# Kernel tuning notes

Hardware: AMD Instinct MI355X
Metric: run time of the kernel (lower is better)

## Reference

```python
import jax, jax.numpy as jnp
import numpy as np

B, P, M, C = 128, 8732, 16, 3
THRESHOLD, NEG_POS_RATIO, ALPHA = 0.5, 3, 1.0


def xy_to_cxcy(xy):
    return jnp.concatenate([(xy[..., 2:] + xy[..., :2]) / 2.0, xy[..., 2:] - xy[..., :2]], axis=-1)


def cxcy_to_xy(cxcy):
    return jnp.concatenate([cxcy[..., :2] - cxcy[..., 2:] / 2.0, cxcy[..., :2] + cxcy[..., 2:] / 2.0], axis=-1)


def cxcy_to_gcxgcy(cxcy, priors_cxcy):
    return jnp.concatenate([
        (cxcy[..., :2] - priors_cxcy[..., :2]) / (priors_cxcy[..., 2:] / 10.0),
        jnp.log(cxcy[..., 2:] / priors_cxcy[..., 2:]) * 5.0], axis=-1)


def jaccard(a, b):
    # a: (M,4) xyxy, b: (P,4) xyxy -> (M,P) IoU
    lt = jnp.maximum(a[:, None, :2], b[None, :, :2])
    rb = jnp.minimum(a[:, None, 2:], b[None, :, 2:])
    wh = jnp.clip(rb - lt, 0.0)
    inter = wh[..., 0] * wh[..., 1]
    area_a = (a[:, 2] - a[:, 0]) * (a[:, 3] - a[:, 1])
    area_b = (b[:, 2] - b[:, 0]) * (b[:, 3] - b[:, 1])
    return inter / (area_a[:, None] + area_b[None, :] - inter)


def setup_inputs() -> dict:
    key = jax.random.key(0)
    k1, k2, k3, k4, k5, k6 = jax.random.split(key, 6)
    predicted_locs = jax.random.normal(k1, (B, P, 4), dtype=jnp.float32)
    predicted_scores = jax.random.normal(k2, (B, P, C), dtype=jnp.float32)
    xy = jax.random.uniform(k3, (B, M, 2), minval=0.0, maxval=0.7)
    wh = jax.random.uniform(k4, (B, M, 2), minval=0.05, maxval=0.3)
    boxes = jnp.concatenate([xy, xy + wh], axis=-1).astype(jnp.float32)
    labels = jax.random.randint(k5, (B, M), 1, 4)  # classes {1,2,3}
    pc = jax.random.uniform(k6, (P, 2), minval=0.0, maxval=1.0)
    pwh = jax.random.uniform(jax.random.fold_in(k6, 1), (P, 2), minval=0.05, maxval=0.5)
    priors_cxcy = jnp.concatenate([pc, pwh], axis=-1).astype(jnp.float32)
    return {"predicted_locs": predicted_locs, "predicted_scores": predicted_scores,
            "boxes": boxes, "labels": labels, "priors_cxcy": priors_cxcy}


def _match_one(boxes_i, labels_i, priors_xy, priors_cxcy):
    ov = jaccard(boxes_i, priors_xy)                # (M, P)
    ov_prior = ov.max(axis=0)                       # best overlap per prior
    obj_prior = ov.argmax(axis=0)                   # best object per prior
    prior_obj = ov.argmax(axis=1)                   # best prior per object
    n_obj = boxes_i.shape[0]
    obj_prior = obj_prior.at[prior_obj].set(jnp.arange(n_obj))
    ov_prior = ov_prior.at[prior_obj].set(1.0)
    lab = jnp.where(ov_prior < THRESHOLD, 0, labels_i[obj_prior])
    tl = cxcy_to_gcxgcy(xy_to_cxcy(boxes_i[obj_prior]), priors_cxcy)
    return tl, lab


def reference(predicted_locs, predicted_scores, boxes, labels, priors_cxcy):
    priors_xy = cxcy_to_xy(priors_cxcy)
    true_locs, true_classes = jax.vmap(_match_one, in_axes=(0, 0, None, None))(
        boxes, labels, priors_xy, priors_cxcy)      # (B,P,4), (B,P)
    positive = true_classes > 0                      # (B,P)
    n_pos = positive.sum(axis=1)                     # (B,)
    n_pos_total = n_pos.sum()

    # localization loss: L1Loss (mean over selected positive elements)
    l1 = jnp.abs(predicted_locs - true_locs).sum(axis=-1)   # (B,P)
    loc_loss = jnp.where(n_pos_total > 0,
                         (l1 * positive).sum() / (4.0 * jnp.maximum(n_pos_total, 1).astype(jnp.float32)),
                         0.0)

    # multi-label one-hot targets (classes 1,2,3; 3 = pair -> targets cols 1&2)
    tc = true_classes.reshape(-1)
    ignore = tc == -1
    pair = tc == 3
    target = jax.nn.one_hot(tc + 1, 5, dtype=predicted_scores.dtype)[:, 1:4]  # (B*P,3)
    target = target.at[:, 1].set(jnp.where(pair, 1.0, target[:, 1]))
    target = target.at[:, 2].set(jnp.where(pair, 1.0, target[:, 2]))

    # BCEWithLogits, summed over classes
    logits = predicted_scores.reshape(-1, C)
    bce = (jnp.logaddexp(0.0, logits) - logits * target).sum(axis=1)  # (B*P,)
    conf_all = jnp.where(ignore, 0.0, bce).reshape(true_classes.shape)  # (B,P)

    conf_pos = (conf_all * positive).sum()
    conf_neg = jnp.where(positive, 0.0, conf_all)
    conf_neg_sorted = -jnp.sort(-conf_neg, axis=1)   # descending per row
    ranks = jnp.arange(P)[None, :]
    hard_neg = ranks < (NEG_POS_RATIO * n_pos)[:, None]
    conf_hard_neg = (conf_neg_sorted * hard_neg).sum()

    conf_loss = (conf_hard_neg + conf_pos) / (1e-10 + n_pos_total.astype(jnp.float32))
    total = conf_loss + ALPHA * loc_loss
    return total, conf_loss, loc_loss, n_pos
```

## Files before the change

kernel.cpp:

```cpp
#include <hip/hip_runtime.h>
#include <hip/hip_fp16.h>
#include <cstdint>
#include <cmath>

#define B_ 128
#define P_ 8732
#define QU_ 2183
#define M_ 16
#define NT 1024
#define NW 16
#define TAIL_ (QU_ - 2*NT)
#define PSTRIDE 9216
#define NFV 144
#define NSLOT 16

__device__ __forceinline__ float softplusf(float x) {
    float e = __builtin_amdgcn_exp2f(fabsf(x) * -1.44269504f);
    return fmaxf(x, 0.0f) + 0.69314718f * __builtin_amdgcn_logf(1.0f + e);
}

__device__ __forceinline__ float wred_sum_f(float v) {
#pragma unroll
    for (int o = 32; o > 0; o >>= 1) v += __shfl_down(v, o, 64);
    return v;
}
__device__ __forceinline__ int wred_sum_i(int v) {
#pragma unroll
    for (int o = 32; o > 0; o >>= 1) v += __shfl_down(v, o, 64);
    return v;
}

__device__ __forceinline__ void phaseD(
    int r, int p, float bv, int bm, float4 pr,
    float x0, float x1, float x2,
    const float* s_boxes, const int* s_labels,
    const float* __restrict__ plocs,
    unsigned short* __restrict__ bcew,
    int& np, float& cp, float& ls)
{
    bool pos = bv >= 0.5f;
    int lab = pos ? s_labels[bm] : 0;
    float t0 = (lab == 0) ? 1.0f : 0.0f;
    float t1 = (lab == 1 || lab == 3) ? 1.0f : 0.0f;
    float t2 = (lab == 2 || lab == 3) ? 1.0f : 0.0f;
    float bce = (softplusf(x0) - x0*t0) + (softplusf(x1) - x1*t1) + (softplusf(x2) - x2*t2);
    float hb = 0.0f;
    if (pos) {
        np++; cp += bce;
        float4 bb = ((const float4*)s_boxes)[bm];
        float cx = (bb.x + bb.z) * 0.5f, cy = (bb.y + bb.w) * 0.5f;
        float w = bb.z - bb.x, hh = bb.w - bb.y;
        float g0 = (cx - pr.x) / (pr.z * 0.1f);
        float g1 = (cy - pr.y) / (pr.w * 0.1f);
        float g2 = logf(w / pr.z) * 5.0f;
        float g3 = logf(hh / pr.w) * 5.0f;
        float4 pl = ((const float4*)plocs)[(size_t)r * P_ + p];
        ls += fabsf(pl.x - g0) + fabsf(pl.y - g1) + fabsf(pl.z - g2) + fabsf(pl.w - g3);
    } else {
        hb = bce;
    }
    bcew[(size_t)r * PSTRIDE + p] = __half_as_ushort(__float2half(hb));
}

__global__ __launch_bounds__(NT) void mbox_match_kernel(
    const float* __restrict__ plocs,
    const float* __restrict__ pscores,
    const float* __restrict__ boxes,
    const int*   __restrict__ labels,
    const float* __restrict__ priors,
    unsigned short* __restrict__ bcew,
    int2* __restrict__ cand,
    float* __restrict__ pcf, float* __restrict__ plc, int* __restrict__ pnp,
    unsigned int* __restrict__ gz)
{
    __shared__ float s_boxes[M_ * 4];
    __shared__ float s_area[M_];
    __shared__ int   s_labels[M_];
    __shared__ unsigned long long s_obj[M_ * NSLOT];
    __shared__ float s_pf[2 * NW];
    __shared__ int   s_pi[NW];

    const int bk = blockIdx.x;
    const int r  = bk >> 2;
    const int q  = bk & 3;
    const int tid = threadIdx.x;
    const int lane = tid & 63;
    const int wid = tid >> 6;
    const int p0 = q * QU_;

    if (bk == 0 && tid < 4) gz[tid] = 0u;

    const int  pA = p0 + tid;
    const int  pB = pA + NT;
    const bool cok = tid < TAIL_;
    const int  pC = cok ? (pB + NT) : pA;

    float4 prA = ((const float4*)priors)[pA];
    float4 prB = ((const float4*)priors)[pB];
    float4 prC = ((const float4*)priors)[pC];

    const float* scA = pscores + ((size_t)r * P_ + pA) * 3;
    const float* scB = pscores + ((size_t)r * P_ + pB) * 3;
    const float* scC = pscores + ((size_t)r * P_ + pC) * 3;
    float xA0 = scA[0], xA1 = scA[1], xA2 = scA[2];
    float xB0 = scB[0], xB1 = scB[1], xB2 = scB[2];
    float xC0 = scC[0], xC1 = scC[1], xC2 = scC[2];

    if (tid < M_ * 4) s_boxes[tid] = boxes[r * M_ * 4 + tid];
    if (tid >= 64 && tid < 64 + M_) s_labels[tid - 64] = labels[r * M_ + (tid - 64)];
    if (tid >= 128 && tid < 128 + M_ * NSLOT)
        s_obj[tid - 128] = (unsigned long long)(unsigned)(16383 - p0);
    __syncthreads();
    if (tid < M_) {
        float x0 = s_boxes[tid*4+0], y0 = s_boxes[tid*4+1];
        float x1 = s_boxes[tid*4+2], y1 = s_boxes[tid*4+3];
        s_area[tid] = (x1 - x0) * (y1 - y0);
    }
    __syncthreads();

    float aX0 = prA.x - prA.z*0.5f, aY0 = prA.y - prA.w*0.5f;
    float aX1 = prA.x + prA.z*0.5f, aY1 = prA.y + prA.w*0.5f;
    float aAr = prA.z * prA.w;
    float bX0 = prB.x - prB.z*0.5f, bY0 = prB.y - prB.w*0.5f;
    float bX1 = prB.x + prB.z*0.5f, bY1 = prB.y + prB.w*0.5f;
    float bAr = prB.z * prB.w;
    float cX0 = prC.x - prC.z*0.5f, cY0 = prC.y - prC.w*0.5f;
    float cX1 = prC.x + prC.z*0.5f, cY1 = prC.y + prC.w*0.5f;
    float cAr = prC.z * prC.w;

    float bvA = -1.0f, bvB = -1.0f, bvC = -1.0f;
    int   bmA = 0,     bmB = 0,     bmC = 0;
    const int slot = lane >> 2;

#pragma unroll
    for (int m = 0; m < M_; ++m) {
        float4 bb = ((const float4*)s_boxes)[m];
        float mar = s_area[m];

        float ltx, lty, rbx, rby, wx, wy, inter;

        ltx = fmaxf(bb.x, aX0); lty = fmaxf(bb.y, aY0);
        rbx = fminf(bb.z, aX1); rby = fminf(bb.w, aY1);
        wx = fmaxf(rbx - ltx, 0.0f); wy = fmaxf(rby - lty, 0.0f);
        inter = wx * wy;
        float ovA = inter * __builtin_amdgcn_rcpf(mar + aAr - inter);

        ltx = fmaxf(bb.x, bX0); lty = fmaxf(bb.y, bY0);
        rbx = fminf(bb.z, bX1); rby = fminf(bb.w, bY1);
        wx = fmaxf(rbx - ltx, 0.0f); wy = fmaxf(rby - lty, 0.0f);
        inter = wx * wy;
        float ovB = inter * __builtin_amdgcn_rcpf(mar + bAr - inter);

        float ovC = -1.0f;
        if (cok) {
            ltx = fmaxf(bb.x, cX0); lty = fmaxf(bb.y, cY0);
            rbx = fminf(bb.z, cX1); rby = fminf(bb.w, cY1);
            wx = fmaxf(rbx - ltx, 0.0f); wy = fmaxf(rby - lty, 0.0f);
            inter = wx * wy;
            ovC = inter * __builtin_amdgcn_rcpf(mar + cAr - inter);
        }

        if (ovA > bvA) { bvA = ovA; bmA = m; }
        if (ovB > bvB) { bvB = ovB; bmB = m; }
        if (ovC > bvC) { bvC = ovC; bmC = m; }

        float v = ovA; int idx = pA;
        if (ovB > v) { v = ovB; idx = pB; }
        if (ovC > v) { v = ovC; idx = pC; }
        if (v > 0.0f) {
            unsigned long long pk =
                ((unsigned long long)__float_as_uint(v) << 32)
                | (unsigned long long)(unsigned)(16383 - idx);
            atomicMax(&s_obj[(m << 4) | slot], pk);
        }
    }

    int np = 0; float cp = 0.0f, ls = 0.0f;
    phaseD(r, pA, bvA, bmA, prA, xA0, xA1, xA2, s_boxes, s_labels,
           plocs, bcew, np, cp, ls);
    phaseD(r, pB, bvB, bmB, prB, xB0, xB1, xB2, s_boxes, s_labels,
           plocs, bcew, np, cp, ls);
    if (cok)
        phaseD(r, pC, bvC, bmC, prC, xC0, xC1, xC2, s_boxes, s_labels,
               plocs, bcew, np, cp, ls);

    cp = wred_sum_f(cp);
    ls = wred_sum_f(ls);
    np = wred_sum_i(np);
    if (lane == 0) { s_pf[wid] = cp; s_pf[NW + wid] = ls; s_pi[wid] = np; }
    __syncthreads();

    if (tid < M_) {
        unsigned long long bb = s_obj[tid << 4];
#pragma unroll
        for (int s = 1; s < NSLOT; ++s) {
            unsigned long long b = s_obj[(tid << 4) | s];
            if (b > bb) bb = b;
        }
        float v = __uint_as_float((unsigned)(bb >> 32));
        int idx = 16383 - (int)(bb & 0xFFFFFFFFull);
        cand[bk * M_ + tid] = make_int2(__float_as_int(v), idx);
    }
    if (tid == 0) {
        float c2 = 0.0f, l2 = 0.0f; int n2 = 0;
#pragma unroll
        for (int w = 0; w < NW; ++w) { c2 += s_pf[w]; l2 += s_pf[NW + w]; n2 += s_pi[w]; }
        pcf[bk] = c2; plc[bk] = l2; pnp[bk] = n2;
    }
}

__global__ __launch_bounds__(64) void mbox_loss_kernel(
    const float* __restrict__ plocs,
    const float* __restrict__ pscores,
    const float* __restrict__ boxes,
    const int*   __restrict__ labels,
    const float* __restrict__ priors,
    const unsigned short* __restrict__ bcew,
    const int2* __restrict__ cand,
    const float* __restrict__ pcf, const float* __restrict__ plc,
    const int* __restrict__ pnp,
    float* __restrict__ out,
    unsigned int* __restrict__ g_cnt,
    float* __restrict__ g_conf, float* __restrict__ g_loc, int* __restrict__ g_np)
{
    __shared__ unsigned short s_fv[PSTRIDE];
    __shared__ float s_boxes[M_ * 4];
    __shared__ int   s_labels[M_];
    __shared__ int   s_po[M_];

    const int r = blockIdx.x;
    const int lane = threadIdx.x;

    {
        const uint4* src = (const uint4*)(bcew + (size_t)r * PSTRIDE);
        uint4* dst = (uint4*)s_fv;
#pragma unroll
        for (int j = 0; j < 18; ++j)
            dst[j * 64 + lane] = src[j * 64 + lane];
    }
    s_boxes[lane] = boxes[r * 64 + lane];
    if (lane < M_) s_labels[lane] = labels[r * M_ + lane];
    if (lane < M_) {
        int2 c = cand[(r * 4) * M_ + lane];
        float v = __int_as_float(c.x); int idx = c.y;
#pragma unroll
        for (int qq = 1; qq < 4; ++qq) {
            int2 c2 = cand[(r * 4 + qq) * M_ + lane];
            float v2 = __int_as_float(c2.x);
            if (v2 > v) { v = v2; idx = c2.y; }
        }
        s_po[lane] = idx;
    }
    __syncthreads();

    for (int p = P_ + lane; p < PSTRIDE; p += 64) s_fv[p] = 0;
    if (lane < M_) s_fv[s_po[lane]] = 0;

    float dcp = 0.0f, dls = 0.0f; int dnp = 0;
    if (lane < M_) {
        const int m = lane;
        const int idx = s_po[m];
        bool owner = true;
        for (int m2 = m + 1; m2 < M_; ++m2)
            if (s_po[m2] == idx) owner = false;
        if (owner) {
            float4 pr = ((const float4*)priors)[idx];
            float pX0 = pr.x - pr.z*0.5f, pY0 = pr.y - pr.w*0.5f;
            float pX1 = pr.x + pr.z*0.5f, pY1 = pr.y + pr.w*0.5f;
            float pAr = pr.z * pr.w;
            float obv = -1.0f; int obm = 0;
#pragma unroll
            for (int mm = 0; mm < M_; ++mm) {
                float4 bb = ((const float4*)s_boxes)[mm];
                float mar = (bb.z - bb.x) * (bb.w - bb.y);
                float ltx = fmaxf(bb.x, pX0), lty = fmaxf(bb.y, pY0);
                float rbx = fminf(bb.z, pX1), rby = fminf(bb.w, pY1);
                float wx = fmaxf(rbx - ltx, 0.0f), wy = fmaxf(rby - lty, 0.0f);
                float inter = wx * wy;
                float ov = inter * __builtin_amdgcn_rcpf(mar + pAr - inter);
                if (ov > obv) { obv = ov; obm = mm; }
            }
            bool oldpos = obv >= 0.5f;
            int  oldobj = obm;

            const float* sc = pscores + ((size_t)r * P_ + idx) * 3;
            float x0 = sc[0], x1 = sc[1], x2 = sc[2];
            float S = softplusf(x0) + softplusf(x1) + softplusf(x2);
            float4 pl = ((const float4*)plocs)[(size_t)r * P_ + idx];
            {
                int lab = s_labels[m];
                float t0 = (lab == 0) ? 1.0f : 0.0f;
                float t1 = (lab == 1 || lab == 3) ? 1.0f : 0.0f;
                float t2 = (lab == 2 || lab == 3) ? 1.0f : 0.0f;
                dcp += S - (x0*t0 + x1*t1 + x2*t2);
                float bx0 = s_boxes[m*4+0], by0 = s_boxes[m*4+1];
                float bx1 = s_boxes[m*4+2], by1 = s_boxes[m*4+3];
                float cx = (bx0+bx1)*0.5f, cy = (by0+by1)*0.5f;
                float w = bx1-bx0, hh = by1-by0;
                float g0 = (cx - pr.x) / (pr.z * 0.1f);
                float g1 = (cy - pr.y) / (pr.w * 0.1f);
                float g2 = logf(w / pr.z) * 5.0f;
                float g3 = logf(hh / pr.w) * 5.0f;
                dls += fabsf(pl.x-g0)+fabsf(pl.y-g1)+fabsf(pl.z-g2)+fabsf(pl.w-g3);
                dnp += 1;
            }
            if (oldpos) {
                int lab = s_labels[oldobj];
                float t0 = (lab == 0) ? 1.0f : 0.0f;
                float t1 = (lab == 1 || lab == 3) ? 1.0f : 0.0f;
                float t2 = (lab == 2 || lab == 3) ? 1.0f : 0.0f;
                dcp -= S - (x0*t0 + x1*t1 + x2*t2);
                float bx0 = s_boxes[oldobj*4+0], by0 = s_boxes[oldobj*4+1];
                float bx1 = s_boxes[oldobj*4+2], by1 = s_boxes[oldobj*4+3];
                float cx = (bx0+bx1)*0.5f, cy = (by0+by1)*0.5f;
                float w = bx1-bx0, hh = by1-by0;
                float g0 = (cx - pr.x) / (pr.z * 0.1f);
                float g1 = (cy - pr.y) / (pr.w * 0.1f);
                float g2 = logf(w / pr.z) * 5.0f;
                float g3 = logf(hh / pr.w) * 5.0f;
                dls -= fabsf(pl.x-g0)+fabsf(pl.y-g1)+fabsf(pl.z-g2)+fabsf(pl.w-g3);
                dnp -= 1;
            }
        }
    }
    dcp = wred_sum_f(dcp);
    dls = wred_sum_f(dls);
    dnp = wred_sum_i(dnp);
    float cp = 0.0f, lsx = 0.0f; int np = 0;
    if (lane == 0) {
        cp = dcp; lsx = dls; np = dnp;
#pragma unroll
        for (int qq = 0; qq < 4; ++qq) {
            cp  += pcf[r * 4 + qq];
            lsx += plc[r * 4 + qq];
            np  += pnp[r * 4 + qq];
        }
    }
    const int npos_row = __shfl(np, 0, 64);

    __syncthreads();

    int fv[NFV];
#pragma unroll
    for (int j = 0; j < 18; ++j) {
        uint4 d = ((const uint4*)s_fv)[j * 64 + lane];
        fv[j*8+0] = (int)(d.x & 0xFFFFu); fv[j*8+1] = (int)(d.x >> 16);
        fv[j*8+2] = (int)(d.y & 0xFFFFu); fv[j*8+3] = (int)(d.y >> 16);
        fv[j*8+4] = (int)(d.z & 0xFFFFu); fv[j*8+5] = (int)(d.z >> 16);
        fv[j*8+6] = (int)(d.w & 0xFFFFu); fv[j*8+7] = (int)(d.w >> 16);
    }

    int k = 3 * npos_row;
    if (k > P_) k = P_;
    float hard_sum = 0.0f;
    if (k > 0) {
        int lo = -1, hi = 0x7C00;
        for (int it = 0; it < 15; ++it) {
            int mid = (lo + hi) >> 1;
            int c = 0;
#pragma unroll
            for (int i = 0; i < NFV; ++i)
                c += (int)__popcll(__ballot(fv[i] > mid));
            if (c < k) hi = mid; else lo = mid;
        }
        int tb = hi;
        float tval = __half2float(__ushort_as_half((unsigned short)tb));
        float lsum = 0.0f; int lcnt = 0;
#pragma unroll
        for (int i = 0; i < NFV; ++i) {
            if (fv[i] > tb) {
                lsum += __half2float(__ushort_as_half((unsigned short)fv[i]));
                lcnt++;
            }
        }
        lsum = wred_sum_f(lsum);
        lcnt = wred_sum_i(lcnt);
        if (lane == 0) hard_sum = lsum + (float)(k - lcnt) * tval;
    }

    if (lane == 0) {
        float conf_row = cp + hard_sum;
        float loc_row  = lsx;
        out[3 + r] = (float)npos_row;
        atomicAdd(g_conf, conf_row);
        atomicAdd(g_loc,  loc_row);
        atomicAdd(g_np,   npos_row);
        __threadfence();
        unsigned int done = atomicAdd(g_cnt, 1u);
        if (done == B_ - 1) {
            float ct = atomicAdd(g_conf, 0.0f);
            float lt = atomicAdd(g_loc,  0.0f);
            int   npt_i = atomicAdd(g_np, 0);
            float npt = (float)npt_i;
            float conf_loss = ct / (1e-10f + npt);
            float loc_loss = (npt_i > 0) ? lt / (4.0f * fmaxf(npt, 1.0f)) : 0.0f;
            out[0] = conf_loss + loc_loss;
            out[1] = conf_loss;
            out[2] = loc_loss;
        }
    }
}

extern "C" void kernel_launch(void* const* d_in, const int* in_sizes, int n_in,
                              void* d_out, int out_size, void* d_ws, size_t ws_size,
                              hipStream_t stream) {
    const float* plocs   = (const float*)d_in[0];
    const float* pscores = (const float*)d_in[1];
    const float* boxes   = (const float*)d_in[2];
    const int*   labels  = (const int*)  d_in[3];
    const float* priors  = (const float*)d_in[4];
    float* out = (float*)d_out;

    char* ws = (char*)d_ws;
    unsigned int* g_cnt  = (unsigned int*)ws;
    float*        g_conf = (float*)(ws + 4);
    float*        g_loc  = (float*)(ws + 8);
    int*          g_np   = (int*)(ws + 12);
    float*        pcf    = (float*)(ws + 64);
    float*        plc    = (float*)(ws + 2112);
    int*          pnp    = (int*)(ws + 4160);
    int2*         cand   = (int2*)(ws + 8192);
    unsigned short* bcew = (unsigned short*)(ws + 73728);

    mbox_match_kernel<<<4 * B_, NT, 0, stream>>>(plocs, pscores, boxes, labels, priors,
                                                 bcew, cand, pcf, plc, pnp,
                                                 (unsigned int*)ws);
    mbox_loss_kernel<<<B_, 64, 0, stream>>>(plocs, pscores, boxes, labels, priors,
                                            bcew, cand, pcf, plc, pnp,
                                            out, g_cnt, g_conf, g_loc, g_np);
}
```

Measured before the change: 136.0 us.

## Widen hard-negative selection kernel to 512 threads with block-level radix count

The loss kernel goes from one 64-lane wavefront per row to 512 threads (8 waves). Each thread holds 18 fp16 BCE values in registers, loaded straight from global memory, so the shared-memory staging buffer is gone. The positive-prior values are zeroed in registers with a computed mask. The 15-step binary threshold search now needs a cross-wave reduction through shared memory and a barrier on every iteration. This cuts the per-thread serial ballot work (144 values per lane down to 18) and raises memory parallelism, at the cost of extra syncthreads per iteration.

```diff
diff --git a/kernel.cpp b/kernel.cpp
--- a/kernel.cpp
+++ b/kernel.cpp
@@ -11,8 +11,11 @@
 #define NW 16
 #define TAIL_ (QU_ - 2*NT)
 #define PSTRIDE 9216
-#define NFV 144
 #define NSLOT 16
+#define K2NT 512
+#define K2NW 8
+#define NU9 9
+#define NFV2 18
 
 __device__ __forceinline__ float softplusf(float x) {
     float e = __builtin_amdgcn_exp2f(fabsf(x) * -1.44269504f);
@@ -209,7 +212,7 @@
     }
 }
 
-__global__ __launch_bounds__(64) void mbox_loss_kernel(
+__global__ __launch_bounds__(K2NT) void mbox_loss_kernel(
     const float* __restrict__ plocs,
     const float* __restrict__ pscores,
     const float* __restrict__ boxes,
@@ -223,132 +226,148 @@
     unsigned int* __restrict__ g_cnt,
     float* __restrict__ g_conf, float* __restrict__ g_loc, int* __restrict__ g_np)
 {
-    __shared__ unsigned short s_fv[PSTRIDE];
     __shared__ float s_boxes[M_ * 4];
     __shared__ int   s_labels[M_];
     __shared__ int   s_po[M_];
+    __shared__ float s_pf[2 * K2NW];
+    __shared__ int   s_pi[K2NW];
+    __shared__ int   s_cnt2[2][K2NW];
+    __shared__ float s_scal[2];
+    __shared__ int   s_npos;
 
     const int r = blockIdx.x;
-    const int lane = threadIdx.x;
-
+    const int tid = threadIdx.x;
+    const int lane = tid & 63;
+    const int wid = tid >> 6;
+
+    int fv[NFV2];
     {
-        const uint4* src = (const uint4*)(bcew + (size_t)r * PSTRIDE);
-        uint4* dst = (uint4*)s_fv;
-#pragma unroll
-        for (int j = 0; j < 18; ++j)
-            dst[j * 64 + lane] = src[j * 64 + lane];
-    }
-    s_boxes[lane] = boxes[r * 64 + lane];
-    if (lane < M_) s_labels[lane] = labels[r * M_ + lane];
-    if (lane < M_) {
-        int2 c = cand[(r * 4) * M_ + lane];
+        const unsigned int* src = (const unsigned int*)(bcew + (size_t)r * PSTRIDE);
+#pragma unroll
+        for (int j = 0; j < NU9; ++j) {
+            int u = j * K2NT + tid;
+            unsigned int d = 0u;
+            if (u < (P_ / 2)) d = src[u];
+            fv[2*j]   = (int)(d & 0xFFFFu);
+            fv[2*j+1] = (int)(d >> 16);
+        }
+    }
+
+    if (tid < M_ * 4) s_boxes[tid] = boxes[r * M_ * 4 + tid];
+    if (tid >= 64 && tid < 64 + M_) s_labels[tid - 64] = labels[r * M_ + (tid - 64)];
+    if (tid >= 128 && tid < 128 + M_) {
+        int m = tid - 128;
+        int2 c = cand[(r * 4) * M_ + m];
         float v = __int_as_float(c.x); int idx = c.y;
 #pragma unroll
         for (int qq = 1; qq < 4; ++qq) {
-            int2 c2 = cand[(r * 4 + qq) * M_ + lane];
+            int2 c2 = cand[(r * 4 + qq) * M_ + m];
             float v2 = __int_as_float(c2.x);
             if (v2 > v) { v = v2; idx = c2.y; }
         }
-        s_po[lane] = idx;
+        s_po[m] = idx;
     }
     __syncthreads();
 
-    for (int p = P_ + lane; p < PSTRIDE; p += 64) s_fv[p] = 0;
-    if (lane < M_) s_fv[s_po[lane]] = 0;
-
-    float dcp = 0.0f, dls = 0.0f; int dnp = 0;
-    if (lane < M_) {
-        const int m = lane;
-        const int idx = s_po[m];
-        bool owner = true;
-        for (int m2 = m + 1; m2 < M_; ++m2)
-            if (s_po[m2] == idx) owner = false;
-        if (owner) {
-            float4 pr = ((const float4*)priors)[idx];
-            float pX0 = pr.x - pr.z*0.5f, pY0 = pr.y - pr.w*0.5f;
-            float pX1 = pr.x + pr.z*0.5f, pY1 = pr.y + pr.w*0.5f;
-            float pAr = pr.z * pr.w;
-            float obv = -1.0f; int obm = 0;
-#pragma unroll
-            for (int mm = 0; mm < M_; ++mm) {
-                float4 bb = ((const float4*)s_boxes)[mm];
-                float mar = (bb.z - bb.x) * (bb.w - bb.y);
-                float ltx = fmaxf(bb.x, pX0), lty = fmaxf(bb.y, pY0);
-                float rbx = fminf(bb.z, pX1), rby = fminf(bb.w, pY1);
-                float wx = fmaxf(rbx - ltx, 0.0f), wy = fmaxf(rby - lty, 0.0f);
-                float inter = wx * wy;
-                float ov = inter * __builtin_amdgcn_rcpf(mar + pAr - inter);
-                if (ov > obv) { obv = ov; obm = mm; }
+    {
+        unsigned int mask = 0u;
+#pragma unroll
+        for (int jj = 0; jj < M_; ++jj) {
+            int rel = s_po[jj] - 2 * tid;
+            if (rel >= 0 && rel < PSTRIDE && (rel & 1022) == 0)
+                mask |= 1u << (((rel >> 10) << 1) | (rel & 1));
+        }
+        if (mask) {
+#pragma unroll
+            for (int i = 0; i < NFV2; ++i)
+                if (mask & (1u << i)) fv[i] = 0;
+        }
+    }
+
+    if (wid == 0) {
+        float dcp = 0.0f, dls = 0.0f; int dnp = 0;
+        if (lane < M_) {
+            const int m = lane;
+            const int idx = s_po[m];
+            bool owner = true;
+            for (int m2 = m + 1; m2 < M_; ++m2)
+                if (s_po[m2] == idx) owner = false;
+            if (owner) {
+                float4 pr = ((const float4*)priors)[idx];
+                float pX0 = pr.x - pr.z*0.5f, pY0 = pr.y - pr.w*0.5f;
+                float pX1 = pr.x + pr.z*0.5f, pY1 = pr.y + pr.w*0.5f;
+                float pAr = pr.z * pr.w;
+                float obv = -1.0f; int obm = 0;
+#pragma unroll
+                for (int mm = 0; mm < M_; ++mm) {
+                    float4 bb = ((const float4*)s_boxes)[mm];
+                    float mar = (bb.z - bb.x) * (bb.w - bb.y);
+                    float ltx = fmaxf(bb.x, pX0), lty = fmaxf(bb.y, pY0);
+                    float rbx = fminf(bb.z, pX1), rby = fminf(bb.w, pY1);
+                    float wx = fmaxf(rbx - ltx, 0.0f), wy = fmaxf(rby - lty, 0.0f);
+                    float inter = wx * wy;
+                    float ov = inter * __builtin_amdgcn_rcpf(mar + pAr - inter);
+                    if (ov > obv) { obv = ov; obm = mm; }
+                }
+                bool oldpos = obv >= 0.5f;
+                int  oldobj = obm;
+
+                const float* sc = pscores + ((size_t)r * P_ + idx) * 3;
+                float x0 = sc[0], x1 = sc[1], x2 = sc[2];
+                float S = softplusf(x0) + softplusf(x1) + softplusf(x2);
+                float4 pl = ((const float4*)plocs)[(size_t)r * P_ + idx];
+                {
+                    int lab = s_labels[m];
+                    float t0 = (lab == 0) ? 1.0f : 0.0f;
+                    float t1 = (lab == 1 || lab == 3) ? 1.0f : 0.0f;
+                    float t2 = (lab == 2 || lab == 3) ? 1.0f : 0.0f;
+                    dcp += S - (x0*t0 + x1*t1 + x2*t2);
+                    float bx0 = s_boxes[m*4+0], by0 = s_boxes[m*4+1];
+                    float bx1 = s_boxes[m*4+2], by1 = s_boxes[m*4+3];
+                    float cx = (bx0+bx1)*0.5f, cy = (by0+by1)*0.5f;
+                    float w = bx1-bx0, hh = by1-by0;
+                    float g0 = (cx - pr.x) / (pr.z * 0.1f);
+                    float g1 = (cy - pr.y) / (pr.w * 0.1f);
+                    float g2 = logf(w / pr.z) * 5.0f;
+                    float g3 = logf(hh / pr.w) * 5.0f;
+                    dls += fabsf(pl.x-g0)+fabsf(pl.y-g1)+fabsf(pl.z-g2)+fabsf(pl.w-g3);
+                    dnp += 1;
+                }
+                if (oldpos) {
+                    int lab = s_labels[oldobj];
+                    float t0 = (lab == 0) ? 1.0f : 0.0f;
+                    float t1 = (lab == 1 || lab == 3) ? 1.0f : 0.0f;
+                    float t2 = (lab == 2 || lab == 3) ? 1.0f : 0.0f;
+                    dcp -= S - (x0*t0 + x1*t1 + x2*t2);
+                    float bx0 = s_boxes[oldobj*4+0], by0 = s_boxes[oldobj*4+1];
+                    float bx1 = s_boxes[oldobj*4+2], by1 = s_boxes[oldobj*4+3];
+                    float cx = (bx0+bx1)*0.5f, cy = (by0+by1)*0.5f;
+                    float w = bx1-bx0, hh = by1-by0;
+                    float g0 = (cx - pr.x) / (pr.z * 0.1f);
+                    float g1 = (cy - pr.y) / (pr.w * 0.1f);
+                    float g2 = logf(w / pr.z) * 5.0f;
+                    float g3 = logf(hh / pr.w) * 5.0f;
+                    dls -= fabsf(pl.x-g0)+fabsf(pl.y-g1)+fabsf(pl.z-g2)+fabsf(pl.w-g3);
+                    dnp -= 1;
+                }
             }
-            bool oldpos = obv >= 0.5f;
-            int  oldobj = obm;
-
-            const float* sc = pscores + ((size_t)r * P_ + idx) * 3;
-            float x0 = sc[0], x1 = sc[1], x2 = sc[2];
-            float S = softplusf(x0) + softplusf(x1) + softplusf(x2);
-            float4 pl = ((const float4*)plocs)[(size_t)r * P_ + idx];
-            {
-                int lab = s_labels[m];
-                float t0 = (lab == 0) ? 1.0f : 0.0f;
-                float t1 = (lab == 1 || lab == 3) ? 1.0f : 0.0f;
-                float t2 = (lab == 2 || lab == 3) ? 1.0f : 0.0f;
-                dcp += S - (x0*t0 + x1*t1 + x2*t2);
-                float bx0 = s_boxes[m*4+0], by0 = s_boxes[m*4+1];
-                float bx1 = s_boxes[m*4+2], by1 = s_boxes[m*4+3];
-                float cx = (bx0+bx1)*0.5f, cy = (by0+by1)*0.5f;
-                float w = bx1-bx0, hh = by1-by0;
-                float g0 = (cx - pr.x) / (pr.z * 0.1f);
-                float g1 = (cy - pr.y) / (pr.w * 0.1f);
-                float g2 = logf(w / pr.z) * 5.0f;
-                float g3 = logf(hh / pr.w) * 5.0f;
-                dls += fabsf(pl.x-g0)+fabsf(pl.y-g1)+fabsf(pl.z-g2)+fabsf(pl.w-g3);
-                dnp += 1;
+        }
+        dcp = wred_sum_f(dcp);
+        dls = wred_sum_f(dls);
+        dnp = wred_sum_i(dnp);
+        if (lane == 0) {
+            float cp = dcp, lsx = dls; int np = dnp;
+#pragma unroll
+            for (int qq = 0; qq < 4; ++qq) {
+                cp  += pcf[r * 4 + qq];
+                lsx += plc[r * 4 + qq];
+                np  += pnp[r * 4 + qq];
             }
-            if (oldpos) {
-                int lab = s_labels[oldobj];
-                float t0 = (lab == 0) ? 1.0f : 0.0f;
-                float t1 = (lab == 1 || lab == 3) ? 1.0f : 0.0f;
-                float t2 = (lab == 2 || lab == 3) ? 1.0f : 0.0f;
-                dcp -= S - (x0*t0 + x1*t1 + x2*t2);
-                float bx0 = s_boxes[oldobj*4+0], by0 = s_boxes[oldobj*4+1];
-                float bx1 = s_boxes[oldobj*4+2], by1 = s_boxes[oldobj*4+3];
-                float cx = (bx0+bx1)*0.5f, cy = (by0+by1)*0.5f;
-                float w = bx1-bx0, hh = by1-by0;
-                float g0 = (cx - pr.x) / (pr.z * 0.1f);
-                float g1 = (cy - pr.y) / (pr.w * 0.1f);
-                float g2 = logf(w / pr.z) * 5.0f;
-                float g3 = logf(hh / pr.w) * 5.0f;
-                dls -= fabsf(pl.x-g0)+fabsf(pl.y-g1)+fabsf(pl.z-g2)+fabsf(pl.w-g3);
-                dnp -= 1;
-            }
-        }
-    }
-    dcp = wred_sum_f(dcp);
-    dls = wred_sum_f(dls);
-    dnp = wred_sum_i(dnp);
-    float cp = 0.0f, lsx = 0.0f; int np = 0;
-    if (lane == 0) {
-        cp = dcp; lsx = dls; np = dnp;
-#pragma unroll
-        for (int qq = 0; qq < 4; ++qq) {
-            cp  += pcf[r * 4 + qq];
-            lsx += plc[r * 4 + qq];
-            np  += pnp[r * 4 + qq];
-        }
-    }
-    const int npos_row = __shfl(np, 0, 64);
-
+            s_scal[0] = cp; s_scal[1] = lsx; s_npos = np;
+        }
+    }
     __syncthreads();
-
-    int fv[NFV];
-#pragma unroll
-    for (int j = 0; j < 18; ++j) {
-        uint4 d = ((const uint4*)s_fv)[j * 64 + lane];
-        fv[j*8+0] = (int)(d.x & 0xFFFFu); fv[j*8+1] = (int)(d.x >> 16);
-        fv[j*8+2] = (int)(d.y & 0xFFFFu); fv[j*8+3] = (int)(d.y >> 16);
-        fv[j*8+4] = (int)(d.z & 0xFFFFu); fv[j*8+5] = (int)(d.z >> 16);
-        fv[j*8+6] = (int)(d.w & 0xFFFFu); fv[j*8+7] = (int)(d.w >> 16);
-    }
+    const int npos_row = s_npos;
 
     int k = 3 * npos_row;
     if (k > P_) k = P_;
@@ -359,15 +378,20 @@
             int mid = (lo + hi) >> 1;
             int c = 0;
 #pragma unroll
-            for (int i = 0; i < NFV; ++i)
-                c += (int)__popcll(__ballot(fv[i] > mid));
-            if (c < k) hi = mid; else lo = mid;
+            for (int i = 0; i < NFV2; ++i) c += (fv[i] > mid) ? 1 : 0;
+            c = wred_sum_i(c);
+            if (lane == 0) s_cnt2[it & 1][wid] = c;
+            __syncthreads();
+            int cnt = 0;
+#pragma unroll
+            for (int w = 0; w < K2NW; ++w) cnt += s_cnt2[it & 1][w];
+            if (cnt < k) hi = mid; else lo = mid;
         }
         int tb = hi;
         float tval = __half2float(__ushort_as_half((unsigned short)tb));
         float lsum = 0.0f; int lcnt = 0;
 #pragma unroll
-        for (int i = 0; i < NFV; ++i) {
+        for (int i = 0; i < NFV2; ++i) {
             if (fv[i] > tb) {
                 lsum += __half2float(__ushort_as_half((unsigned short)fv[i]));
                 lcnt++;
@@ -375,12 +399,19 @@
         }
         lsum = wred_sum_f(lsum);
         lcnt = wred_sum_i(lcnt);
-        if (lane == 0) hard_sum = lsum + (float)(k - lcnt) * tval;
-    }
-
-    if (lane == 0) {
-        float conf_row = cp + hard_sum;
-        float loc_row  = lsx;
+        if (lane == 0) { s_pf[wid] = lsum; s_pi[wid] = lcnt; }
+        __syncthreads();
+        if (tid == 0) {
+            float sv = 0.0f; int sc2 = 0;
+#pragma unroll
+            for (int w = 0; w < K2NW; ++w) { sv += s_pf[w]; sc2 += s_pi[w]; }
+            hard_sum = sv + (float)(k - sc2) * tval;
+        }
+    }
+
+    if (tid == 0) {
+        float conf_row = s_scal[0] + hard_sum;
+        float loc_row  = s_scal[1];
         out[3 + r] = (float)npos_row;
         atomicAdd(g_conf, conf_row);
         atomicAdd(g_loc,  loc_row);
@@ -425,7 +456,7 @@
     mbox_match_kernel<<<4 * B_, NT, 0, stream>>>(plocs, pscores, boxes, labels, priors,
                                                  bcew, cand, pcf, plc, pnp,
                                                  (unsigned int*)ws);
-    mbox_loss_kernel<<<B_, 64, 0, stream>>>(plocs, pscores, boxes, labels, priors,
-                                            bcew, cand, pcf, plc, pnp,
-                                            out, g_cnt, g_conf, g_loc, g_np);
-}
+    mbox_loss_kernel<<<B_, K2NT, 0, stream>>>(plocs, pscores, boxes, labels, priors,
+                                              bcew, cand, pcf, plc, pnp,
+                                              out, g_cnt, g_conf, g_loc, g_np);
+}
```

Result: faster. 115.9 us (-14.8%).
